# Kernel optimization log

Hardware: AMD Instinct MI355X
Metric: run time of the kernel (lower is better)

The kernel has to match this reference:

```python
import jax, jax.numpy as jnp
import numpy as np


def _run_lstm(x, W, U, b, mask=None):
    """Keras-style LSTM returning final hidden state.
    x: [N, T, D] float; W: [D, 4u]; U: [u, 4u]; b: [4u]; mask: [N, T] bool or None.
    Gate order i, f, g(c), o as in Keras. Masked steps carry state through.
    """
    N, T, D = x.shape
    units = U.shape[0]
    xt = jnp.transpose(x, (1, 0, 2))  # [T, N, D]
    if mask is not None:
        mt = jnp.transpose(mask, (1, 0))[:, :, None]  # [T, N, 1]
        xs = (xt, mt)
    else:
        xs = xt

    def step(carry, inp):
        h, c = carry
        if mask is not None:
            x_t, m = inp
        else:
            x_t = inp
        z = x_t @ W + h @ U + b  # [N, 4u]
        i, f, g, o = jnp.split(z, 4, axis=-1)
        i = jax.nn.sigmoid(i)
        f = jax.nn.sigmoid(f)
        g = jnp.tanh(g)
        o = jax.nn.sigmoid(o)
        c_new = f * c + i * g
        h_new = o * jnp.tanh(c_new)
        if mask is not None:
            h_new = jnp.where(m, h_new, h)
            c_new = jnp.where(m, c_new, c)
        return (h_new, c_new), None

    h0 = jnp.zeros((N, units), dtype=x.dtype)
    c0 = jnp.zeros((N, units), dtype=x.dtype)
    (hT, _), _ = jax.lax.scan(step, (h0, c0), xs)
    return hT


def setup_inputs() -> dict:
    key = jax.random.key(0)
    ks = jax.random.split(key, 10)
    B, T, S, D = 256, 256, 20, 1
    U1, U2 = 32, 24  # inner / outer LSTM units
    sc = 0.1
    x = jax.random.normal(ks[0], (B, T, S, D), dtype=jnp.float32)
    lengths = jax.random.randint(ks[1], (B,), 1, T + 1, dtype=jnp.int32)
    Wi = jax.random.normal(ks[2], (D, 4 * U1), dtype=jnp.float32) * sc
    Ui = jax.random.normal(ks[3], (U1, 4 * U1), dtype=jnp.float32) * sc
    bi = jnp.zeros((4 * U1,), dtype=jnp.float32)
    Wo = jax.random.normal(ks[4], (U1, 4 * U2), dtype=jnp.float32) * sc
    Uo = jax.random.normal(ks[5], (U2, 4 * U2), dtype=jnp.float32) * sc
    bo = jnp.zeros((4 * U2,), dtype=jnp.float32)
    Wd = jax.random.normal(ks[6], (U2, 1), dtype=jnp.float32) * sc
    bd = jnp.zeros((1,), dtype=jnp.float32)
    return {"x": x, "lengths": lengths, "Wi": Wi, "Ui": Ui, "bi": bi,
            "Wo": Wo, "Uo": Uo, "bo": bo, "Wd": Wd, "bd": bd}


def reference(x, lengths, Wi, Ui, bi, Wo, Uo, bo, Wd, bd):
    B, T, S, D = x.shape
    # TimeDistributed(LSTM(32)): run inner LSTM over each outer step (inference, dropout off)
    rows = x.reshape(B * T, S, D)
    h_inner = _run_lstm(rows, Wi, Ui, bi)          # [B*T, 32]
    feats = h_inner.reshape(B, T, -1)              # [B, T, 32]
    # Outer LSTM(24) with ragged-length mask (Keras mask semantics: carry state)
    mask = jnp.arange(T)[None, :] < lengths[:, None]  # [B, T]
    h_outer = _run_lstm(feats, Wo, Uo, bo, mask)   # [B, 24]
    # Dense sigmoid head
    return jax.nn.sigmoid(h_outer @ Wd + bd)       # [B, 1]
```

## Files before the change

kernel.cpp:

```cpp
#include <hip/hip_runtime.h>

#define B_  256
#define T_  256
#define S_  20
#define U1  32
#define G1  128
#define U2  24
#define G2  96
#define NT  16

typedef __attribute__((ext_vector_type(8))) short short8;
typedef __attribute__((ext_vector_type(4))) float f32x4;

__device__ __forceinline__ float sigmoidf_(float x) {
    return __builtin_amdgcn_rcpf(1.0f + __builtin_amdgcn_exp2f(x * -1.44269504f));
}
__device__ __forceinline__ float tanhf_fast(float x) {
    return 1.0f - 2.0f * __builtin_amdgcn_rcpf(1.0f + __builtin_amdgcn_exp2f(x * 2.88539008f));
}

__device__ __forceinline__ unsigned short f2bf(float a) {
    unsigned int u = __float_as_uint(a);
    u += 0x7FFFu + ((u >> 16) & 1u);
    return (unsigned short)(u >> 16);
}
__device__ __forceinline__ unsigned int pack2bf(float a, float b) {
    unsigned int ua = __float_as_uint(a); ua += 0x7FFFu + ((ua >> 16) & 1u);
    unsigned int ub = __float_as_uint(b); ub += 0x7FFFu + ((ub >> 16) & 1u);
    return (ua >> 16) | (ub & 0xFFFF0000u);
}
union frag_u { short8 v; unsigned int u[4]; };
union h2x  { unsigned int u32; _Float16 h[2]; };

__global__ __attribute__((amdgpu_flat_work_group_size(512, 512)))
__attribute__((amdgpu_waves_per_eu(2, 2)))
void fused_kernel(
    const float* __restrict__ x,
    const int*   __restrict__ lengths,
    const float* __restrict__ Wi,
    const float* __restrict__ Ui,
    const float* __restrict__ bi,
    const float* __restrict__ Wo,
    const float* __restrict__ Uo,
    const float* __restrict__ bo,
    const float* __restrict__ Wd,
    const float* __restrict__ bd,
    float* __restrict__ out)
{
    __shared__ __align__(16) _Float16      Pl[T_][G2];
    __shared__ __align__(16) unsigned short hbb[8][16][40];
    __shared__ unsigned int flags[NT];
    const int b    = blockIdx.x;
    const int len  = lengths[b];
    const int tid  = threadIdx.x;
    const int w    = __builtin_amdgcn_readfirstlane(tid >> 6);
    const int lane = tid & 63;
    const int q    = lane >> 4;
    const int n    = lane & 15;

    if (tid < NT) flags[tid] = 0;
    __syncthreads();

    frag_u Bui[8];
#pragma unroll
    for (int tt = 0; tt < 8; ++tt)
#pragma unroll
        for (int k2 = 0; k2 < 4; ++k2)
            Bui[tt].u[k2] = pack2bf(Ui[(8 * q + 2 * k2) * G1 + 16 * tt + n],
                                    Ui[(8 * q + 2 * k2 + 1) * G1 + 16 * tt + n]);
    frag_u Bwo[6];
#pragma unroll
    for (int tt = 0; tt < 6; ++tt)
#pragma unroll
        for (int k2 = 0; k2 < 4; ++k2)
            Bwo[tt].u[k2] = pack2bf(Wo[(8 * q + 2 * k2) * G2 + 16 * tt + n],
                                    Wo[(8 * q + 2 * k2 + 1) * G2 + 16 * tt + n]);
    float bi_l[8], Wi_l[8], bo_l[6];
#pragma unroll
    for (int tt = 0; tt < 8; ++tt) { bi_l[tt] = bi[16 * tt + n]; Wi_l[tt] = Wi[16 * tt + n]; }
#pragma unroll
    for (int tt = 0; tt < 6; ++tt) bo_l[tt] = bo[16 * tt + n];
    int pcol[6];
#pragma unroll
    for (int tt = 0; tt < 6; ++tt) {
        const int col = 16 * tt + n;
        const int g = col / 24;
        pcol[tt] = (col - 24 * g) * 4 + g;
    }

    int tl[3]; int ntl;
    if (w == 0)      { tl[0] = 0; tl[1] = 0; tl[2] = 0; ntl = 1; }
    else if (w == 1) { tl[0] = 1; tl[1] = 8; tl[2] = 9; ntl = 3; }
    else             { tl[0] = w; tl[1] = w + 8; tl[2] = 0; ntl = 2; }

#pragma unroll 1
    for (int i = 0; i < ntl; ++i) {
        const int tile = tl[i];
        const int wt0  = tile * 16;
        if (wt0 >= len) break;

        const float* xr = x + (size_t)(b * T_ + wt0 + 4 * q) * S_;
        float c[2][4];
#pragma unroll
        for (int uh = 0; uh < 2; ++uh)
#pragma unroll
            for (int r = 0; r < 4; ++r) c[uh][r] = 0.0f;

        float xc[4];
#pragma unroll
        for (int r = 0; r < 4; ++r) xc[r] = xr[r * S_];

        {
            f32x4 acc[8];
#pragma unroll
            for (int tt = 0; tt < 8; ++tt)
#pragma unroll
                for (int r = 0; r < 4; ++r)
                    acc[tt][r] = bi_l[tt] + xc[r] * Wi_l[tt];
#pragma unroll
            for (int uh = 0; uh < 2; ++uh)
#pragma unroll
                for (int r = 0; r < 4; ++r) {
                    const float iv = sigmoidf_(acc[0 + uh][r]);
                    const float fv = sigmoidf_(acc[2 + uh][r]);
                    const float gv = tanhf_fast(acc[4 + uh][r]);
                    const float ov = sigmoidf_(acc[6 + uh][r]);
                    c[uh][r] = fv * c[uh][r] + iv * gv;
                    hbb[w][4 * q + r][n + 16 * uh] = f2bf(ov * tanhf_fast(c[uh][r]));
                }
        }
#pragma unroll
        for (int r = 0; r < 4; ++r) xc[r] = xr[r * S_ + 1];

#pragma unroll 1
        for (int s = 1; s < S_; ++s) {
            const int sn = (s + 1 < S_) ? s + 1 : S_ - 1;
            float xnx[4];
#pragma unroll
            for (int r = 0; r < 4; ++r) xnx[r] = xr[r * S_ + sn];

            f32x4 acc[8];
#pragma unroll
            for (int tt = 0; tt < 8; ++tt)
#pragma unroll
                for (int r = 0; r < 4; ++r)
                    acc[tt][r] = bi_l[tt] + xc[r] * Wi_l[tt];

            const short8 A = *(const short8*)&hbb[w][n][8 * q];
#pragma unroll
            for (int tt = 0; tt < 8; ++tt)
                acc[tt] = __builtin_amdgcn_mfma_f32_16x16x32_bf16(A, Bui[tt].v, acc[tt], 0, 0, 0);

#pragma unroll
            for (int uh = 0; uh < 2; ++uh)
#pragma unroll
                for (int r = 0; r < 4; ++r) {
                    const float iv = sigmoidf_(acc[0 + uh][r]);
                    const float fv = sigmoidf_(acc[2 + uh][r]);
                    const float gv = tanhf_fast(acc[4 + uh][r]);
                    const float ov = sigmoidf_(acc[6 + uh][r]);
                    c[uh][r] = fv * c[uh][r] + iv * gv;
                    hbb[w][4 * q + r][n + 16 * uh] = f2bf(ov * tanhf_fast(c[uh][r]));
                }
#pragma unroll
            for (int r = 0; r < 4; ++r) xc[r] = xnx[r];
        }

        {
            const short8 A = *(const short8*)&hbb[w][n][8 * q];
            f32x4 accp[6];
#pragma unroll
            for (int tt = 0; tt < 6; ++tt) {
#pragma unroll
                for (int r = 0; r < 4; ++r) accp[tt][r] = bo_l[tt];
                accp[tt] = __builtin_amdgcn_mfma_f32_16x16x32_bf16(A, Bwo[tt].v, accp[tt], 0, 0, 0);
            }
#pragma unroll
            for (int r = 0; r < 4; ++r) {
                const int tr = wt0 + 4 * q + r;
#pragma unroll
                for (int tt = 0; tt < 6; ++tt)
                    Pl[tr][pcol[tt]] = (_Float16)accp[tt][r];
            }
        }
        __hip_atomic_store(&flags[tile], 1u, __ATOMIC_RELEASE, __HIP_MEMORY_SCOPE_WORKGROUP);
    }

    if (w != 0) return;

    const int half = lane >> 5;
    const int sub  = lane & 31;
    const int u    = (sub < U2) ? sub : U2 - 1;

    float wA[U2], wB[U2];
#pragma unroll
    for (int k = 0; k < U2; ++k) {
        wA[k] = Uo[k * G2 + (2 * half) * U2 + u];
        wB[k] = Uo[k * G2 + (2 * half + 1) * U2 + u];
    }

    auto ldrow = [&](int t) -> f32x4 {
        const uint2 raw = *reinterpret_cast<const uint2*>(&Pl[t][4 * u]);
        h2x a, c2; a.u32 = raw.x; c2.u32 = raw.y;
        f32x4 r;
        r[0] = (float)a.h[0];  r[1] = (float)a.h[1];
        r[2] = (float)c2.h[0]; r[3] = (float)c2.h[1];
        return r;
    };

    f32x4 cur = ldrow(0);
    float cu, hu;
    {
        const float ig = sigmoidf_(cur[0]);
        const float gg = tanhf_fast(cur[2]);
        const float og = sigmoidf_(cur[3]);
        cu = ig * gg;
        hu = og * tanhf_fast(cu);
    }
    int wtile = 0;
    f32x4 nxt = ldrow((1 < len) ? 1 : 0);

#pragma unroll 1
    for (int t = 1; t < len; ++t) {
        const int tn = (t + 1 < len) ? (t + 1) : (len - 1);
        const int ttile = tn >> 4;
        if (ttile != wtile) {
            while (__hip_atomic_load(&flags[ttile], __ATOMIC_ACQUIRE,
                                     __HIP_MEMORY_SCOPE_WORKGROUP) == 0u)
                __builtin_amdgcn_s_sleep(1);
            wtile = ttile;
        }
        const f32x4 pf = ldrow(tn);

        float hk[U2];
#pragma unroll
        for (int k = 0; k < U2; ++k)
            hk[k] = __int_as_float(__builtin_amdgcn_readlane(__float_as_int(hu), k));

        const float pA = half ? nxt[2] : nxt[0];
        const float pB = half ? nxt[3] : nxt[1];
        float a0 = pA, a1 = 0.0f, a2 = 0.0f, a3 = 0.0f;
        float b0 = pB, b1 = 0.0f, b2 = 0.0f, b3 = 0.0f;
#pragma unroll
        for (int k = 0; k < U2; k += 4) {
            a0 += hk[k]     * wA[k];     b0 += hk[k]     * wB[k];
            a1 += hk[k + 1] * wA[k + 1]; b1 += hk[k + 1] * wB[k + 1];
            a2 += hk[k + 2] * wA[k + 2]; b2 += hk[k + 2] * wB[k + 2];
            a3 += hk[k + 3] * wA[k + 3]; b3 += hk[k + 3] * wB[k + 3];
        }
        const float zA = (a0 + a1) + (a2 + a3);
        const float zB = (b0 + b1) + (b2 + b3);
        const float oA = __shfl_xor(zA, 32);
        const float oB = __shfl_xor(zB, 32);

        const float z_i = half ? oA : zA;
        const float z_f = half ? oB : zB;
        const float z_g = half ? zA : oA;
        const float z_o = half ? zB : oB;

        const float ig = sigmoidf_(z_i);
        const float fg = sigmoidf_(z_f);
        const float gg = tanhf_fast(z_g);
        const float og = sigmoidf_(z_o);
        cu = fg * cu + ig * gg;
        hu = og * tanhf_fast(cu);

        nxt = pf;
    }

    float acc = bd[0];
#pragma unroll
    for (int k = 0; k < U2; ++k)
        acc += __int_as_float(__builtin_amdgcn_readlane(__float_as_int(hu), k)) * Wd[k];
    if (lane == 0) out[b] = sigmoidf_(acc);
}

extern "C" void kernel_launch(void* const* d_in, const int* in_sizes, int n_in,
                              void* d_out, int out_size, void* d_ws, size_t ws_size,
                              hipStream_t stream) {
    const float* x       = (const float*)d_in[0];
    const int*   lengths = (const int*)  d_in[1];
    const float* Wi      = (const float*)d_in[2];
    const float* Ui      = (const float*)d_in[3];
    const float* bi      = (const float*)d_in[4];
    const float* Wo      = (const float*)d_in[5];
    const float* Uo      = (const float*)d_in[6];
    const float* bo      = (const float*)d_in[7];
    const float* Wd      = (const float*)d_in[8];
    const float* bd      = (const float*)d_in[9];
    float* out = (float*)d_out;

    fused_kernel<<<dim3(B_), dim3(512), 0, stream>>>(
        x, lengths, Wi, Ui, bi, Wo, Uo, bo, Wd, bd, out);
}
```

Before: 163.6 us.

## Remap outer LSTM lanes to pairs with DPP swap, packed FMA, and wave priorities

The serial outer recurrence now maps each unit to an adjacent lane pair instead of lanes 32 apart. This replaces the cross-half __shfl_xor (an LDS permute) with a cheap DPP quad swap and uses packed two-wide float FMAs for the gate dot products. Wave priorities are also set so the producer waves run at high priority during the first tile, then wave 0 (the recurrence wave) is favoured. The aim is to shorten the per-timestep latency on the critical serial path. It adds scheduling complexity and may not help if the loop is bound by readlanes.

```diff
diff --git a/kernel.cpp b/kernel.cpp
--- a/kernel.cpp
+++ b/kernel.cpp
@@ -11,12 +11,17 @@
 
 typedef __attribute__((ext_vector_type(8))) short short8;
 typedef __attribute__((ext_vector_type(4))) float f32x4;
+typedef __attribute__((ext_vector_type(2))) float f32x2;
 
 __device__ __forceinline__ float sigmoidf_(float x) {
     return __builtin_amdgcn_rcpf(1.0f + __builtin_amdgcn_exp2f(x * -1.44269504f));
 }
 __device__ __forceinline__ float tanhf_fast(float x) {
     return 1.0f - 2.0f * __builtin_amdgcn_rcpf(1.0f + __builtin_amdgcn_exp2f(x * 2.88539008f));
+}
+__device__ __forceinline__ float dpp_xor1(float x) {
+    return __int_as_float(__builtin_amdgcn_update_dpp(
+        0, __float_as_int(x), 0xB1, 0xF, 0xF, true));
 }
 
 __device__ __forceinline__ unsigned short f2bf(float a) {
@@ -61,6 +66,8 @@
     if (tid < NT) flags[tid] = 0;
     __syncthreads();
 
+    if (w <= 3) __builtin_amdgcn_s_setprio(2);
+
     frag_u Bui[8];
 #pragma unroll
     for (int tt = 0; tt < 8; ++tt)
@@ -184,41 +191,52 @@
             }
         }
         __hip_atomic_store(&flags[tile], 1u, __ATOMIC_RELEASE, __HIP_MEMORY_SCOPE_WORKGROUP);
+        if (i == 0) {
+            if (w == 0) __builtin_amdgcn_s_setprio(1);
+            else        __builtin_amdgcn_s_setprio(0);
+        }
     }
 
     if (w != 0) return;
 
-    const int half = lane >> 5;
-    const int sub  = lane & 31;
-    const int u    = (sub < U2) ? sub : U2 - 1;
-
-    float wA[U2], wB[U2];
+    const int p = lane & 1;
+    const int u = (lane < 2 * U2) ? (lane >> 1) : (U2 - 1);
+    const int cA = p ? (2 * U2 + u) : u;
+    const int cB = p ? (3 * U2 + u) : (U2 + u);
+
+    f32x2 w2_[U2];
 #pragma unroll
     for (int k = 0; k < U2; ++k) {
-        wA[k] = Uo[k * G2 + (2 * half) * U2 + u];
-        wB[k] = Uo[k * G2 + (2 * half + 1) * U2 + u];
-    }
-
-    auto ldrow = [&](int t) -> f32x4 {
+        w2_[k].x = Uo[k * G2 + cA];
+        w2_[k].y = Uo[k * G2 + cB];
+    }
+
+    auto ldrow2 = [&](int t) -> f32x2 {
         const uint2 raw = *reinterpret_cast<const uint2*>(&Pl[t][4 * u]);
-        h2x a, c2; a.u32 = raw.x; c2.u32 = raw.y;
-        f32x4 r;
-        r[0] = (float)a.h[0];  r[1] = (float)a.h[1];
-        r[2] = (float)c2.h[0]; r[3] = (float)c2.h[1];
+        h2x s_; s_.u32 = p ? raw.y : raw.x;
+        f32x2 r; r.x = (float)s_.h[0]; r.y = (float)s_.h[1];
         return r;
     };
 
-    f32x4 cur = ldrow(0);
-    float cu, hu;
+    float cu = 0.0f, hu;
     {
-        const float ig = sigmoidf_(cur[0]);
-        const float gg = tanhf_fast(cur[2]);
-        const float og = sigmoidf_(cur[3]);
-        cu = ig * gg;
+        const f32x2 z0 = ldrow2(0);
+        const float zA = z0.x, zB = z0.y;
+        const float swA = dpp_xor1(zA);
+        const float swB = dpp_xor1(zB);
+        const float z_i = p ? swA : zA;
+        const float z_f = p ? swB : zB;
+        const float z_g = p ? zA : swA;
+        const float z_o = p ? zB : swB;
+        const float ig = sigmoidf_(z_i);
+        const float fg = sigmoidf_(z_f);
+        const float gg = tanhf_fast(z_g);
+        const float og = sigmoidf_(z_o);
+        cu = fg * cu + ig * gg;
         hu = og * tanhf_fast(cu);
     }
     int wtile = 0;
-    f32x4 nxt = ldrow((1 < len) ? 1 : 0);
+    f32x2 nxt = ldrow2((1 < len) ? 1 : 0);
 
 #pragma unroll 1
     for (int t = 1; t < len; ++t) {
@@ -230,33 +248,31 @@
                 __builtin_amdgcn_s_sleep(1);
             wtile = ttile;
         }
-        const f32x4 pf = ldrow(tn);
+        const f32x2 pf = ldrow2(tn);
 
         float hk[U2];
 #pragma unroll
         for (int k = 0; k < U2; ++k)
-            hk[k] = __int_as_float(__builtin_amdgcn_readlane(__float_as_int(hu), k));
-
-        const float pA = half ? nxt[2] : nxt[0];
-        const float pB = half ? nxt[3] : nxt[1];
-        float a0 = pA, a1 = 0.0f, a2 = 0.0f, a3 = 0.0f;
-        float b0 = pB, b1 = 0.0f, b2 = 0.0f, b3 = 0.0f;
+            hk[k] = __int_as_float(__builtin_amdgcn_readlane(__float_as_int(hu), 2 * k));
+
+        f32x2 ab0 = nxt;
+        f32x2 ab1 = {0.0f, 0.0f}, ab2 = {0.0f, 0.0f}, ab3 = {0.0f, 0.0f};
 #pragma unroll
         for (int k = 0; k < U2; k += 4) {
-            a0 += hk[k]     * wA[k];     b0 += hk[k]     * wB[k];
-            a1 += hk[k + 1] * wA[k + 1]; b1 += hk[k + 1] * wB[k + 1];
-            a2 += hk[k + 2] * wA[k + 2]; b2 += hk[k + 2] * wB[k + 2];
-            a3 += hk[k + 3] * wA[k + 3]; b3 += hk[k + 3] * wB[k + 3];
-        }
-        const float zA = (a0 + a1) + (a2 + a3);
-        const float zB = (b0 + b1) + (b2 + b3);
-        const float oA = __shfl_xor(zA, 32);
-        const float oB = __shfl_xor(zB, 32);
-
-        const float z_i = half ? oA : zA;
-        const float z_f = half ? oB : zB;
-        const float z_g = half ? zA : oA;
-        const float z_o = half ? zB : oB;
+            ab0 += w2_[k]     * hk[k];
+            ab1 += w2_[k + 1] * hk[k + 1];
+            ab2 += w2_[k + 2] * hk[k + 2];
+            ab3 += w2_[k + 3] * hk[k + 3];
+        }
+        const f32x2 zz = (ab0 + ab1) + (ab2 + ab3);
+        const float zA = zz.x, zB = zz.y;
+
+        const float swA = dpp_xor1(zA);
+        const float swB = dpp_xor1(zB);
+        const float z_i = p ? swA : zA;
+        const float z_f = p ? swB : zB;
+        const float z_g = p ? zA : swA;
+        const float z_o = p ? zB : swB;
 
         const float ig = sigmoidf_(z_i);
         const float fg = sigmoidf_(z_f);
@@ -271,7 +287,7 @@
     float acc = bd[0];
 #pragma unroll
     for (int k = 0; k < U2; ++k)
-        acc += __int_as_float(__builtin_amdgcn_readlane(__float_as_int(hu), k)) * Wd[k];
+        acc += __int_as_float(__builtin_amdgcn_readlane(__float_as_int(hu), 2 * k)) * Wd[k];
     if (lane == 0) out[b] = sigmoidf_(acc);
 }
 
```

Result: faster. 159.4 us (-2.6%).
